# Performance work log

Measured on AMD Instinct MI355X. Metric: run time of the kernel, lower is better.

## Reference

```python
import jax, jax.numpy as jnp
import numpy as np

B, H, W = 8, 256, 256
GH, GW = 32, 32          # orig_grid_shape, = img / 2^3 after three stride-2 convs
N_STEPS = 6              # masks_num: r_x_total=3, r_y_total=3, alternating dim_stride
C_FEAT = 64
N_MASK = 4               # 4 shifted supervoxel masks summed in setup
DN = ('NHWC', 'HWIO', 'NHWC')
# deconves_importances[r_x-1]; r_x sequence over steps = 1,1,2,2,3,3
LOSS_W = (0.1, 0.1, 0.5, 0.5, 1.0, 1.0)


def _conv(x, w, b, strides=(1, 1)):
    return jax.lax.conv_general_dilated(x, w, strides, 'SAME', dimension_numbers=DN) + b


def _trio(x, w, b, strides=(1, 1)):
    # Conv_trio: conv + channel norm + gelu
    y = _conv(x, w, b, strides)
    mu = jnp.mean(y, axis=-1, keepdims=True)
    var = jnp.var(y, axis=-1, keepdims=True)
    y = (y - mu) * jax.lax.rsqrt(var + 1e-6)
    return jax.nn.gelu(y)


def setup_inputs() -> dict:
    key = jax.random.key(0)
    ks = jax.random.split(key, 8)
    s = 0.05
    w1 = jax.random.normal(ks[0], (3, 3, 1, 16), jnp.float32) * s
    w2 = jax.random.normal(ks[1], (3, 3, 16, 16), jnp.float32) * s
    w3 = jax.random.normal(ks[2], (3, 3, 16, 32), jnp.float32) * s
    w4 = jax.random.normal(ks[3], (3, 3, 32, C_FEAT), jnp.float32) * s
    up_w = jax.random.normal(ks[4], (3, 3, C_FEAT, C_FEAT), jnp.float32) * s
    mask_w = jax.random.normal(ks[5], (3, 3, C_FEAT, N_MASK), jnp.float32) * s
    b1 = jnp.zeros((16,)); b2 = jnp.zeros((16,)); b3 = jnp.zeros((32,))
    b4 = jnp.zeros((C_FEAT,)); up_b = jnp.zeros((C_FEAT,)); mask_b = jnp.zeros((N_MASK,))
    # initial supervoxel masks: sum of 4 shifted checkerboards -> per-cell grid ids
    xs = jnp.arange(GH) % 2
    ys = jnp.arange(GW) % 2
    ids = (xs[:, None] + 2 * ys[None, :]).astype(jnp.float32)  # [GH,GW] in {0,1,2,3}
    masks0 = jnp.broadcast_to(ids[None, :, :, None], (B, GH, GW, 1))
    image = jax.random.normal(ks[6], (B, H, W, 1), jnp.float32)
    return {"image": image, "dynamic_cfg": 0,
            "w1": w1, "b1": b1, "w2": w2, "b2": b2, "w3": w3, "b3": b3,
            "w4": w4, "b4": b4, "up_w": up_w, "up_b": up_b,
            "mask_w": mask_w, "mask_b": mask_b, "masks0": masks0}


def reference(image, dynamic_cfg, w1, b1, w2, b2, w3, b3, w4, b4,
              up_w, up_b, mask_w, mask_b, masks0):
    # encoder: Conv_trio(16) -> (16,s2) -> (32,s2) -> (64,s2)
    x = _trio(image, w1, b1)
    x = _trio(x, w2, b2, (2, 2))
    x = _trio(x, w3, b3, (2, 2))
    deconv_multi = _trio(x, w4, b4, (2, 2))  # [B,32,32,64]
    masks = masks0
    losses = jnp.zeros((1,), image.dtype)
    offsets = jnp.arange(N_MASK, dtype=image.dtype)
    for i in range(N_STEPS):  # fixed, structurally distinct resolutions
        dim = i % 2  # alternating dim_stride as in r_x_r_y_dim_stride
        strides = (2, 1) if dim == 0 else (1, 2)
        deconv_multi = jax.nn.gelu(
            jax.lax.conv_transpose(deconv_multi, up_w, strides, 'SAME',
                                   dimension_numbers=DN) + up_b)
        probs = jax.nn.softmax(_conv(deconv_multi, mask_w, mask_b), axis=-1)  # [B,h,w,4]
        masks = jnp.repeat(masks, 2, axis=dim + 1)
        masks = masks + 0.25 * jnp.sum(probs * offsets, axis=-1, keepdims=True)
        h, w_ = deconv_multi.shape[1], deconv_multi.shape[2]
        img_ds = image.reshape(B, h, H // h, w_, W // w_, 1).mean(axis=(2, 4))
        recon = jnp.sum(probs * offsets, axis=-1, keepdims=True) / 3.0
        entropy = -jnp.sum(probs * jnp.log(probs + 1e-8), axis=-1)
        losses = losses + LOSS_W[i] * (jnp.mean(entropy) + jnp.mean((recon - img_ds) ** 2))
    return losses, masks
```

## Files before the change

### kernel.cpp

```cpp
#include <hip/hip_runtime.h>
#include <hip/hip_bf16.h>
#include <math.h>

typedef __hip_bfloat16 bf16;
typedef float f32x4 __attribute__((ext_vector_type(4)));
typedef __bf16 bf16x8 __attribute__((ext_vector_type(8)));

#define DEV __device__ __forceinline__

DEV float to_f(float v){ return v; }
DEV float to_f(bf16 v){ return __bfloat162float(v); }
DEV bf16 f2b(float v){ return __float2bfloat16(v); }
DEV unsigned short b2u(bf16 v){ return __builtin_bit_cast(unsigned short, v); }

DEV float gelu_f(float x){
  float z = 1.5957691216057308f*(x + 0.044715f*x*x*x);
  float e = __expf(-z);
  return x * __builtin_amdgcn_rcpf(1.0f + e);
}

DEV bf16x8 load_frag(const bf16* p, bool ok){
  uint4 u = make_uint4(0u,0u,0u,0u);
  if (ok) u = *(const uint4*)p;
  return __builtin_bit_cast(bf16x8, u);
}

DEV f32x4 mfma16(bf16x8 a, uint4 b, f32x4 c){
  return __builtin_amdgcn_mfma_f32_16x16x32_bf16(a, __builtin_bit_cast(bf16x8, b), c, 0, 0, 0);
}

DEV int swz8(int blk, int n){
  return (blk & 7) * (n >> 3) + (blk >> 3);
}

DEV void dma16(const void* g, void* l){
  __builtin_amdgcn_global_load_lds(
      (const __attribute__((address_space(1))) unsigned int*)g,
      (__attribute__((address_space(3))) unsigned int*)l,
      16, 0, 0);
}

#define NSLOT 64

template<typename TIN, int CIN, int COUT, int SUB, int STRIDE, int HI, int WI>
__global__ void trio_kernel(const TIN* __restrict__ in, const float* __restrict__ w,
                            const float* __restrict__ bias, bf16* __restrict__ out){
  constexpr int HO = HI/STRIDE, WO = WI/STRIDE;
  constexpr int CO_PER = COUT/SUB;
  int gtid = blockIdx.x*blockDim.x + threadIdx.x;
  int sub = gtid % SUB;
  int pix = gtid / SUB;
  int b = pix / (HO*WO); int rem = pix % (HO*WO);
  int y = rem / WO, x = rem % WO;

  float acc[CO_PER];
  #pragma unroll
  for (int j=0;j<CO_PER;j++) acc[j]=0.f;

  for (int ky=0;ky<3;ky++){
    int iy = (STRIDE==1) ? (y+ky-1) : (2*y+ky);
    if (iy<0 || iy>=HI) continue;
    for (int kx=0;kx<3;kx++){
      int ix = (STRIDE==1) ? (x+kx-1) : (2*x+kx);
      if (ix<0 || ix>=WI) continue;
      const TIN* ip = in + ((size_t)(b*HI+iy)*WI+ix)*CIN;
      const float* wp = w + ((ky*3+kx)*CIN)*COUT + sub*CO_PER;
      #pragma unroll 4
      for (int ci=0; ci<CIN; ci++){
        float a = to_f(ip[ci]);
        const float4* w4 = (const float4*)(wp + (size_t)ci*COUT);
        #pragma unroll
        for (int j=0;j<CO_PER/4;j++){
          float4 ww = w4[j];
          acc[4*j+0] += a*ww.x; acc[4*j+1] += a*ww.y;
          acc[4*j+2] += a*ww.z; acc[4*j+3] += a*ww.w;
        }
      }
    }
  }

  float s1=0.f, s2=0.f;
  #pragma unroll
  for (int j=0;j<CO_PER;j++){
    acc[j] += bias[sub*CO_PER+j];
    s1 += acc[j]; s2 += acc[j]*acc[j];
  }
  #pragma unroll
  for (int off=1; off<SUB; off<<=1){
    s1 += __shfl_xor(s1,off,64);
    s2 += __shfl_xor(s2,off,64);
  }
  float mu  = s1*(1.0f/COUT);
  float var = s2*(1.0f/COUT) - mu*mu;
  float sc  = rsqrtf(var + 1e-6f);

  bf16* op = out + (size_t)pix*COUT + sub*CO_PER;
  #pragma unroll
  for (int j=0;j<CO_PER;j++) op[j] = f2b(gelu_f((acc[j]-mu)*sc));
}


template<int COUT>
__global__ void repack_c16(const float* __restrict__ w, bf16* __restrict__ bp){
  constexpr int NT = COUT/16;
  int v = blockIdx.x*256 + threadIdx.x;
  if (v >= 5*NT*64*8) return;
  int j = v & 7; int lane = (v>>3)&63; int idx = v>>9;
  int nt = idx % NT; int P = idx / NT;
  int m = lane & 15, quad = lane >> 4;
  int tp = quad >> 1;
  int ci = (quad & 1)*8 + j;
  int tap = 2*P + tp;
  int co = nt*16 + m;
  bp[v] = (tap < 9) ? f2b(w[((size_t)tap*16 + ci)*COUT + co]) : f2b(0.0f);
}

__global__ void repack_c32(const float* __restrict__ w, bf16* __restrict__ bp){
  int v = blockIdx.x*256 + threadIdx.x;
  if (v >= 9*4*64*8) return;
  int j = v & 7; int lane = (v>>3)&63; int idx = v>>9;
  int nt = idx & 3; int tap = idx >> 2;
  int m = lane & 15, quad = lane >> 4;
  int ci = quad*8 + j;
  int co = nt*16 + m;
  bp[v] = f2b(w[((size_t)tap*32 + ci)*64 + co]);
}

template<int CIN, int COUT, int HI, int WI>
__global__ void trio_mfma(const bf16* __restrict__ in, const bf16* __restrict__ bpack,
                          const float* __restrict__ bias, bf16* __restrict__ out){
  constexpr int HO = HI/2, WO = WI/2, NT = COUT/16;
  constexpr int TPR = WO/16;
  int lane = threadIdx.x & 63, wv = threadIdx.x >> 6;
  int wtile = blockIdx.x*4 + wv;
  int m = lane & 15, quad = lane >> 4;

  int x0 = (wtile % TPR)*16;
  int oy = (wtile / TPR) % HO;
  int b  = wtile / (TPR*HO);

  const uint4* bp4 = (const uint4*)bpack;

  f32x4 acc[NT];
  #pragma unroll
  for (int nt=0;nt<NT;nt++) acc[nt] = (f32x4){0.f,0.f,0.f,0.f};

  if constexpr (CIN == 32){
    #pragma unroll
    for (int tap=0; tap<9; tap++){
      int ky = tap/3, kx = tap%3;
      int iy = 2*oy + ky;
      int ix = 2*(x0 + m) + kx;
      bool ok = (iy < HI) && (ix < WI);
      bf16x8 a = load_frag(in + ((size_t)(b*HI+iy)*WI + ix)*32 + quad*8, ok);
      #pragma unroll
      for (int nt=0;nt<NT;nt++)
        acc[nt] = mfma16(a, bp4[(tap*NT+nt)*64 + lane], acc[nt]);
    }
  } else {
    #pragma unroll
    for (int P=0; P<5; P++){
      int tap = 2*P + (quad >> 1);
      int ky = tap/3, kx = tap - ky*3;
      int iy = 2*oy + ky;
      int ix = 2*(x0 + m) + kx;
      bool ok = (tap < 9) && (iy < HI) && (ix < WI);
      bf16x8 a = load_frag(in + ((size_t)(b*HI+iy)*WI + ix)*16 + (quad&1)*8, ok);
      #pragma unroll
      for (int nt=0;nt<NT;nt++)
        acc[nt] = mfma16(a, bp4[(P*NT+nt)*64 + lane], acc[nt]);
    }
  }

  float av[NT][4];
  float s1[4] = {0.f,0.f,0.f,0.f}, s2[4] = {0.f,0.f,0.f,0.f};
  #pragma unroll
  for (int nt=0;nt<NT;nt++){
    float bv = bias[nt*16 + m];
    #pragma unroll
    for (int r=0;r<4;r++){
      float v = acc[nt][r] + bv;
      av[nt][r] = v;
      s1[r] += v; s2[r] += v*v;
    }
  }
  #pragma unroll
  for (int r=0;r<4;r++){
    #pragma unroll
    for (int off=1; off<16; off<<=1){
      s1[r] += __shfl_xor(s1[r], off, 64);
      s2[r] += __shfl_xor(s2[r], off, 64);
    }
  }
  #pragma unroll
  for (int r=0;r<4;r++){
    float mu  = s1[r]*(1.0f/COUT);
    float var = s2[r]*(1.0f/COUT) - mu*mu;
    float sc  = rsqrtf(var + 1e-6f);
    size_t px = ((size_t)(b*HO + oy))*WO + x0 + quad*4 + r;
    #pragma unroll
    for (int nt=0;nt<NT;nt++)
      out[px*COUT + nt*16 + m] = f2b(gelu_f((av[nt][r]-mu)*sc));
  }
}

__global__ void repack_up(const float* __restrict__ w, bf16* __restrict__ bp){
  int v = blockIdx.x*256 + threadIdx.x;
  if (v >= 9*2*4*64*8) return;
  int j = v & 7; int lane = (v>>3)&63; int nt = (v>>9)&3; int c = (v>>11)&1; int tap = v>>12;
  int ci = c*32 + (lane>>4)*8 + j;
  int co = (lane&15)*4 + nt;
  bp[v] = f2b(w[(tap*64+ci)*64 + co]);
}

__global__ void repack_mask(const float* __restrict__ w, bf16* __restrict__ bp){
  int v = blockIdx.x*256 + threadIdx.x;
  if (v >= 9*2*64*8) return;
  int j = v & 7; int lane = (v>>3)&63; int c = (v>>9)&1; int tap = v>>10;
  int ci = c*32 + (lane>>4)*8 + j;
  int n = lane & 15;
  bp[v] = (n < 4) ? f2b(w[(tap*64+ci)*4 + n]) : f2b(0.0f);
}

template<int HI, int WI>
__global__ void upconv_dim0(const bf16* __restrict__ in, const bf16* __restrict__ bpack,
                            const float* __restrict__ upb, bf16* __restrict__ out){
  constexpr int HO = 2*HI, WO = WI, XT = WI/32;
  int lane = threadIdx.x & 63, wv = threadIdx.x >> 6;
  int wtile = swz8(blockIdx.x, gridDim.x)*4 + wv;
  int m = lane & 15, quad = lane >> 4;

  int x0 = (wtile % XT)*32;
  int o  = (wtile / XT) % HO;
  int b  = wtile / (XT*HO);

  int q = o >> 1;
  int stk[2], stq[2]; int nst;
  if (o & 1){ stk[0]=1; stq[0]=q; nst=1; }
  else {
    nst = 0;
    if (q >= 1){ stk[0]=0; stq[0]=q-1; nst=1; }
    stk[nst]=2; stq[nst]=q; nst++;
  }

  f32x4 acc[2][4];
  #pragma unroll
  for (int t=0;t<2;t++)
    #pragma unroll
    for (int nt=0;nt<4;nt++) acc[t][nt] = (f32x4){0.f,0.f,0.f,0.f};

  const uint4* bp4 = (const uint4*)bpack;

  #pragma unroll 1
  for (int s=0; s<nst; s++){
    int kyt = stk[s];
    const bf16* rowp = in + ((size_t)(b*HI+stq[s])*WI)*64 + quad*8;
    #pragma unroll
    for (int ut=0; ut<3; ut++){
      #pragma unroll
      for (int c=0;c<2;c++){
        int ix0 = x0 + m - 1 + ut;
        int ix1 = ix0 + 16;
        bf16x8 a0 = load_frag(rowp + (size_t)ix0*64 + c*32, ix0>=0 && ix0<WI);
        bf16x8 a1 = load_frag(rowp + (size_t)ix1*64 + c*32, ix1>=0 && ix1<WI);
        #pragma unroll
        for (int nt=0;nt<4;nt++){
          uint4 Bq = bp4[(((kyt*3+ut)*2+c)*4+nt)*64 + lane];
          acc[0][nt] = mfma16(a0, Bq, acc[0][nt]);
          acc[1][nt] = mfma16(a1, Bq, acc[1][nt]);
        }
      }
    }
  }

  float4 bv = *(const float4*)(upb + m*4);
  size_t rowbase = ((size_t)b*HO + o)*WO;
  #pragma unroll
  for (int t=0;t<2;t++){
    #pragma unroll
    for (int r=0;r<4;r++){
      int p = x0 + t*16 + quad*4 + r;
      float g0 = gelu_f(acc[t][0][r] + bv.x);
      float g1 = gelu_f(acc[t][1][r] + bv.y);
      float g2 = gelu_f(acc[t][2][r] + bv.z);
      float g3 = gelu_f(acc[t][3][r] + bv.w);
      unsigned int lo = (unsigned int)b2u(f2b(g0)) | ((unsigned int)b2u(f2b(g1))<<16);
      unsigned int hi = (unsigned int)b2u(f2b(g2)) | ((unsigned int)b2u(f2b(g3))<<16);
      *(uint2*)(out + (rowbase + p)*64 + m*4) = make_uint2(lo,hi);
    }
  }
}

template<int HI, int WI>
__global__ void __launch_bounds__(256,2)
upconv_dim0_bs(const bf16* __restrict__ in, const bf16* __restrict__ bpack,
               const float* __restrict__ upb, bf16* __restrict__ out){
  constexpr int HO = 2*HI, WO = WI, XT = WI/32;
  __shared__ __align__(16) uint4 Bsh[4608];
  int tid = threadIdx.x, lane = tid & 63, wv = tid >> 6;
  int wtile = swz8(blockIdx.x, gridDim.x)*4 + wv;
  int m = lane & 15, quad = lane >> 4;

  int x0 = (wtile % XT)*32;
  int o  = (wtile / XT) % HO;
  int b  = wtile / (XT*HO);

  {
    const uint4* gp = (const uint4*)bpack;
    #pragma unroll
    for (int k=0;k<18;k++){
      int base = (wv*18 + k)*64;
      dma16(gp + base + lane, Bsh + base);
    }
  }

  int q = o >> 1;
  int stk[2], stq[2]; int nst;
  if (o & 1){ stk[0]=1; stq[0]=q; nst=1; }
  else {
    nst = 0;
    if (q >= 1){ stk[0]=0; stq[0]=q-1; nst=1; }
    stk[nst]=2; stq[nst]=q; nst++;
  }

  f32x4 acc[2][4];
  #pragma unroll
  for (int t=0;t<2;t++)
    #pragma unroll
    for (int nt=0;nt<4;nt++) acc[t][nt] = (f32x4){0.f,0.f,0.f,0.f};

  asm volatile("s_waitcnt vmcnt(0)" ::: "memory");
  __syncthreads();

  #pragma unroll 1
  for (int s=0; s<nst; s++){
    int kyt = stk[s];
    const bf16* rowp = in + ((size_t)(b*HI+stq[s])*WI)*64 + quad*8;
    #pragma unroll
    for (int ut=0; ut<3; ut++){
      #pragma unroll
      for (int c=0;c<2;c++){
        int ix0 = x0 + m - 1 + ut;
        int ix1 = ix0 + 16;
        bf16x8 a0 = load_frag(rowp + (size_t)ix0*64 + c*32, ix0>=0 && ix0<WI);
        bf16x8 a1 = load_frag(rowp + (size_t)ix1*64 + c*32, ix1>=0 && ix1<WI);
        #pragma unroll
        for (int nt=0;nt<4;nt++){
          uint4 Bq = Bsh[(((kyt*3+ut)*2+c)*4+nt)*64 + lane];
          acc[0][nt] = mfma16(a0, Bq, acc[0][nt]);
          acc[1][nt] = mfma16(a1, Bq, acc[1][nt]);
        }
      }
    }
  }

  float4 bv = *(const float4*)(upb + m*4);
  size_t rowbase = ((size_t)b*HO + o)*WO;
  #pragma unroll
  for (int t=0;t<2;t++){
    #pragma unroll
    for (int r=0;r<4;r++){
      int p = x0 + t*16 + quad*4 + r;
      float g0 = gelu_f(acc[t][0][r] + bv.x);
      float g1 = gelu_f(acc[t][1][r] + bv.y);
      float g2 = gelu_f(acc[t][2][r] + bv.z);
      float g3 = gelu_f(acc[t][3][r] + bv.w);
      unsigned int lo = (unsigned int)b2u(f2b(g0)) | ((unsigned int)b2u(f2b(g1))<<16);
      unsigned int hi = (unsigned int)b2u(f2b(g2)) | ((unsigned int)b2u(f2b(g3))<<16);
      *(uint2*)(out + (rowbase + p)*64 + m*4) = make_uint2(lo,hi);
    }
  }
}

template<int HI, int WI>
__global__ void upconv_dim1(const bf16* __restrict__ in, const bf16* __restrict__ bpack,
                            const float* __restrict__ upb, bf16* __restrict__ out){
  constexpr int HO = HI, WO = 2*WI, QT = WI/16;
  int lane = threadIdx.x & 63, wv = threadIdx.x >> 6;
  int wtile = swz8(blockIdx.x, gridDim.x)*4 + wv;
  int m = lane & 15, quad = lane >> 4;

  int q0 = (wtile % QT)*16;
  int y  = (wtile / QT) % HI;
  int b  = wtile / (QT*HI);

  f32x4 ae[4], ao[4];
  #pragma unroll
  for (int nt=0;nt<4;nt++){ ae[nt]=(f32x4){0.f,0.f,0.f,0.f}; ao[nt]=(f32x4){0.f,0.f,0.f,0.f}; }

  const uint4* bp4 = (const uint4*)bpack;

  #pragma unroll 1
  for (int ky=0; ky<3; ky++){
    int iy = y + ky - 1;
    if (iy < 0 || iy >= HI) continue;
    const bf16* rowp = in + ((size_t)(b*HI+iy)*WI)*64 + quad*8;
    #pragma unroll
    for (int c=0;c<2;c++){
      int qa = q0 + m;
      bf16x8 Au = load_frag(rowp + (size_t)qa*64 + c*32, true);
      bf16x8 As = load_frag(rowp + (size_t)(qa-1)*64 + c*32, qa >= 1);
      #pragma unroll
      for (int nt=0;nt<4;nt++){
        uint4 B0 = bp4[(((ky*3+0)*2+c)*4+nt)*64 + lane];
        uint4 B1 = bp4[(((ky*3+1)*2+c)*4+nt)*64 + lane];
        uint4 B2 = bp4[(((ky*3+2)*2+c)*4+nt)*64 + lane];
        ae[nt] = mfma16(As, B0, ae[nt]);
        ae[nt] = mfma16(Au, B2, ae[nt]);
        ao[nt] = mfma16(Au, B1, ao[nt]);
      }
    }
  }

  float4 bv = *(const float4*)(upb + m*4);
  size_t rowbase = ((size_t)b*HO + y)*WO;
  #pragma unroll
  for (int r=0;r<4;r++){
    int qq = q0 + quad*4 + r;
    {
      float g0 = gelu_f(ae[0][r] + bv.x);
      float g1 = gelu_f(ae[1][r] + bv.y);
      float g2 = gelu_f(ae[2][r] + bv.z);
      float g3 = gelu_f(ae[3][r] + bv.w);
      unsigned int lo = (unsigned int)b2u(f2b(g0)) | ((unsigned int)b2u(f2b(g1))<<16);
      unsigned int hi = (unsigned int)b2u(f2b(g2)) | ((unsigned int)b2u(f2b(g3))<<16);
      *(uint2*)(out + (rowbase + 2*qq)*64 + m*4) = make_uint2(lo,hi);
    }
    {
      float g0 = gelu_f(ao[0][r] + bv.x);
      float g1 = gelu_f(ao[1][r] + bv.y);
      float g2 = gelu_f(ao[2][r] + bv.z);
      float g3 = gelu_f(ao[3][r] + bv.w);
      unsigned int lo = (unsigned int)b2u(f2b(g0)) | ((unsigned int)b2u(f2b(g1))<<16);
      unsigned int hi = (unsigned int)b2u(f2b(g2)) | ((unsigned int)b2u(f2b(g3))<<16);
      *(uint2*)(out + (rowbase + 2*qq+1)*64 + m*4) = make_uint2(lo,hi);
    }
  }
}

template<int HI, int WI>
__global__ void __launch_bounds__(256,2)
upconv_dim1_bs(const bf16* __restrict__ in, const bf16* __restrict__ bpack,
               const float* __restrict__ upb, bf16* __restrict__ out){
  constexpr int HO = HI, WO = 2*WI, QT = WI/16;
  __shared__ __align__(16) uint4 Bsh[4608];
  int tid = threadIdx.x, lane = tid & 63, wv = tid >> 6;
  int wtile = swz8(blockIdx.x, gridDim.x)*4 + wv;
  int m = lane & 15, quad = lane >> 4;

  int q0 = (wtile % QT)*16;
  int y  = ((wtile / QT) % (HI/2)) * 2;
  int b  = wtile / (QT*(HI/2));

  {
    const uint4* gp = (const uint4*)bpack;
    #pragma unroll
    for (int k=0;k<18;k++){
      int base = (wv*18 + k)*64;
      dma16(gp + base + lane, Bsh + base);
    }
  }

  int qa = q0 + m;

  bf16x8 Afr[4][2][2];
  #pragma unroll
  for (int i4=0;i4<4;i4++){
    int iy = y + i4 - 1;
    bool ok = (iy>=0) && (iy<HI);
    const bf16* rowp = in + ((size_t)(b*HI+iy)*WI)*64 + quad*8;
    #pragma unroll
    for (int c=0;c<2;c++){
      Afr[i4][c][0] = load_frag(rowp + (size_t)qa*64 + c*32, ok);
      Afr[i4][c][1] = load_frag(rowp + (size_t)(qa-1)*64 + c*32, ok && qa >= 1);
    }
  }

  asm volatile("s_waitcnt vmcnt(0)" ::: "memory");
  __syncthreads();

  f32x4 ae[2][4], ao[2][4];
  #pragma unroll
  for (int r=0;r<2;r++)
    #pragma unroll
    for (int nt=0;nt<4;nt++){ ae[r][nt]=(f32x4){0.f,0.f,0.f,0.f}; ao[r][nt]=(f32x4){0.f,0.f,0.f,0.f}; }

  #pragma unroll
  for (int ky=0; ky<3; ky++){
    #pragma unroll
    for (int c=0;c<2;c++){
      #pragma unroll
      for (int nt=0;nt<4;nt++){
        uint4 B0 = Bsh[(((ky*3+0)*2+c)*4+nt)*64 + lane];
        uint4 B1 = Bsh[(((ky*3+1)*2+c)*4+nt)*64 + lane];
        uint4 B2 = Bsh[(((ky*3+2)*2+c)*4+nt)*64 + lane];
        #pragma unroll
        for (int r=0;r<2;r++){
          ae[r][nt] = mfma16(Afr[ky+r][c][1], B0, ae[r][nt]);
          ae[r][nt] = mfma16(Afr[ky+r][c][0], B2, ae[r][nt]);
          ao[r][nt] = mfma16(Afr[ky+r][c][0], B1, ao[r][nt]);
        }
      }
    }
  }

  float4 bv = *(const float4*)(upb + m*4);
  #pragma unroll
  for (int r2=0;r2<2;r2++){
    size_t rowbase = ((size_t)b*HO + y + r2)*WO;
    #pragma unroll
    for (int r=0;r<4;r++){
      int qq = q0 + quad*4 + r;
      {
        float g0 = gelu_f(ae[r2][0][r] + bv.x);
        float g1 = gelu_f(ae[r2][1][r] + bv.y);
        float g2 = gelu_f(ae[r2][2][r] + bv.z);
        float g3 = gelu_f(ae[r2][3][r] + bv.w);
        unsigned int lo = (unsigned int)b2u(f2b(g0)) | ((unsigned int)b2u(f2b(g1))<<16);
        unsigned int hi = (unsigned int)b2u(f2b(g2)) | ((unsigned int)b2u(f2b(g3))<<16);
        *(uint2*)(out + (rowbase + 2*qq)*64 + m*4) = make_uint2(lo,hi);
      }
      {
        float g0 = gelu_f(ao[r2][0][r] + bv.x);
        float g1 = gelu_f(ao[r2][1][r] + bv.y);
        float g2 = gelu_f(ao[r2][2][r] + bv.z);
        float g3 = gelu_f(ao[r2][3][r] + bv.w);
        unsigned int lo = (unsigned int)b2u(f2b(g0)) | ((unsigned int)b2u(f2b(g1))<<16);
        unsigned int hi = (unsigned int)b2u(f2b(g2)) | ((unsigned int)b2u(f2b(g3))<<16);
        *(uint2*)(out + (rowbase + 2*qq+1)*64 + m*4) = make_uint2(lo,hi);
      }
    }
  }
}

template<int STEP, int DIM, int HH, int WW, int TILES>
__global__ void maskloss_mfma(const bf16* __restrict__ feat, const bf16* __restrict__ mpack,
                              const float* __restrict__ mb, const float* __restrict__ img,
                              const float* __restrict__ masks_in, float* __restrict__ masks_out,
                              float* __restrict__ accbuf){
  __shared__ float llog[4][64][4];
  __shared__ float red[4][2];
  int lane = threadIdx.x & 63;
  int wv   = threadIdx.x >> 6;
  int wtile = swz8(blockIdx.x, gridDim.x)*4 + wv;
  int m = lane & 15, quad = lane >> 4;

  constexpr int TPR = WW/(16*TILES);
  int x0 = (wtile % TPR)*(16*TILES);
  int y  = (wtile / TPR) % HH;
  int b  = wtile / (TPR*HH);

  const uint4* bp4 = (const uint4*)mpack;

  #pragma unroll 1
  for (int t=0; t<TILES; t++){
    f32x4 acc4 = (f32x4){0.f,0.f,0.f,0.f};
    #pragma unroll
    for (int c=0;c<2;c++){
      bf16x8 afr[9];
      #pragma unroll
      for (int ky=0; ky<3; ky++){
        int iy = y + ky - 1;
        bool rowok = (iy >= 0) && (iy < HH);
        const bf16* rowp = feat + ((size_t)(b*HH+iy)*WW)*64 + quad*8 + c*32;
        #pragma unroll
        for (int kx=0; kx<3; kx++){
          int ix = x0 + t*16 + m + kx - 1;
          bool ok = rowok && (ix >= 0) && (ix < WW);
          afr[ky*3+kx] = load_frag(rowp + (size_t)ix*64, ok);
        }
      }
      #pragma unroll
      for (int tap=0; tap<9; tap++){
        uint4 bb = bp4[(tap*2+c)*64 + lane];
        acc4 = mfma16(afr[tap], bb, acc4);
      }
    }
    if (m < 4){
      #pragma unroll
      for (int r=0;r<4;r++) llog[wv][t*16 + quad*4 + r][m] = acc4[r] + mb[m];
    }
  }
  __syncthreads();

  float ent = 0.f, mse = 0.f;
  if (lane < 16*TILES){
    int p = lane; int xx = x0 + p;
    float l0 = llog[wv][p][0], l1 = llog[wv][p][1];
    float l2 = llog[wv][p][2], l3 = llog[wv][p][3];
    float mx = fmaxf(fmaxf(l0,l1), fmaxf(l2,l3));
    float d0=l0-mx, d1=l1-mx, d2=l2-mx, d3=l3-mx;
    float e0=__expf(d0), e1=__expf(d1), e2=__expf(d2), e3=__expf(d3);
    float S = e0+e1+e2+e3;
    float inv = __builtin_amdgcn_rcpf(S);
    float sval = (e1 + 2.f*e2 + 3.f*e3)*inv;

    constexpr int HM = (DIM==0)? HH/2 : HH;
    constexpr int WM = (DIM==0)? WW : WW/2;
    int my = (DIM==0)? (y>>1) : y;
    int mxi = (DIM==1)? (xx>>1) : xx;
    float mv = masks_in[((size_t)b*HM + my)*WM + mxi];
    masks_out[((size_t)b*HH + y)*WW + xx] = mv + 0.25f*sval;

    ent = __logf(S) - (e0*d0 + e1*d1 + e2*d2 + e3*d3)*inv;

    constexpr int FH = 256/HH, FW = 256/WW;
    float isum = 0.f;
    const float* ib = img + ((size_t)b*256 + y*FH)*256 + xx*FW;
    #pragma unroll
    for (int dy=0; dy<FH; dy++)
      #pragma unroll
      for (int dx=0; dx<FW; dx++) isum += ib[dy*256+dx];
    float img_ds = isum * (1.0f/(FH*FW));
    float d = sval*(1.0f/3.0f) - img_ds;
    mse = d*d;
  }

  #pragma unroll
  for (int off=1; off<64; off<<=1){
    ent += __shfl_xor(ent, off, 64);
    mse += __shfl_xor(mse, off, 64);
  }
  if (lane == 0){ red[wv][0] = ent; red[wv][1] = mse; }
  __syncthreads();
  if (threadIdx.x == 0){
    float e  = red[0][0] + red[1][0] + red[2][0] + red[3][0];
    float ms = red[0][1] + red[1][1] + red[2][1] + red[3][1];
    int slot = blockIdx.x & (NSLOT-1);
    atomicAdd(accbuf + (2*STEP  )*NSLOT + slot, e);
    atomicAdd(accbuf + (2*STEP+1)*NSLOT + slot, ms);
  }
}

template<int STEP, int DIM, int HH, int WW, int ROWS>
__global__ void maskloss_lds(const bf16* __restrict__ feat, const bf16* __restrict__ mpack,
                             const float* __restrict__ mb, const float* __restrict__ img,
                             const float* __restrict__ masks_in, float* __restrict__ masks_out,
                             float* __restrict__ accbuf){
  constexpr int NBrow = WW/64;
  constexpr int PITCH = 9216;
  constexpr int NR = ROWS + 2;
  constexpr int WPR = 4/ROWS;
  __shared__ __align__(16) char smem[NR*PITCH];
  __shared__ float llog[4][ROWS][16][4];
  __shared__ float red[4][2];
  int tid = threadIdx.x;
  int lane = tid & 63, wv = tid >> 6;
  int bi = swz8(blockIdx.x, gridDim.x);
  int x0 = (bi % NBrow)*64;
  int y0 = ((bi / NBrow) % (HH/ROWS)) * ROWS;
  int b  = bi / (NBrow*(HH/ROWS));
  int m = lane & 15, quad = lane >> 4;
  int lanesw = ((lane ^ (lane>>3)) << 4);

  int r_w   = wv / WPR;
  int xbase = (wv % WPR) * (16*ROWS);
  int yw    = y0 + r_w;

  for (int k = wv; k < NR*9; k += 4){
    int r = k/9, coff = (k%9)*1024;
    int iy = y0 + r - 1;
    if (iy < 0 || iy >= HH) continue;
    const char* g = (const char*)(feat + ((size_t)(b*HH+iy)*WW + x0 - 1)*64)
                    + coff + lanesw;
    dma16(g, smem + r*PITCH + coff);
  }
  asm volatile("s_waitcnt vmcnt(0)" ::: "memory");
  __syncthreads();
  if (x0 == 0 && tid < 32*NR)
    ((float*)(smem + (tid>>5)*PITCH))[tid & 31] = 0.f;
  if (x0 + 64 == WW && tid >= 128 && tid < 128 + 32*NR){
    int t = tid - 128;
    ((float*)(smem + (t>>5)*PITCH + 65*128))[t & 31] = 0.f;
  }
  __syncthreads();

  const uint4* bp4 = (const uint4*)mpack;
  #pragma unroll
  for (int t=0; t<ROWS; t++){
    f32x4 accA = (f32x4){0.f,0.f,0.f,0.f};
    f32x4 accB = (f32x4){0.f,0.f,0.f,0.f};
    #pragma unroll
    for (int ky=0; ky<3; ky++){
      int iyw = yw + ky - 1;
      if (iyw < 0 || iyw >= HH) continue;
      const char* rowl = smem + (size_t)(r_w + ky)*PITCH;
      #pragma unroll
      for (int kx=0; kx<3; kx++){
        int lp = xbase + t*16 + m + kx;
        const char* pl = rowl + (size_t)lp*128;
        int xw = (lp & 7) << 4;
        bf16x8 a0 = __builtin_bit_cast(bf16x8, *(const uint4*)(pl + ((quad*16     ) ^ xw)));
        bf16x8 a1 = __builtin_bit_cast(bf16x8, *(const uint4*)(pl + ((quad*16 + 64) ^ xw)));
        uint4 b0 = bp4[((ky*3+kx)*2+0)*64 + lane];
        uint4 b1 = bp4[((ky*3+kx)*2+1)*64 + lane];
        accA = mfma16(a0, b0, accA);
        accB = mfma16(a1, b1, accB);
      }
    }
    if (m < 4){
      #pragma unroll
      for (int r=0;r<4;r++) llog[wv][t][quad*4+r][m] = accA[r] + accB[r] + mb[m];
    }
  }
  __syncthreads();

  float ent = 0.f, mse = 0.f;
  if (lane < 16*ROWS){
    int t = lane >> 4;
    int p = lane & 15;
    int xx = x0 + xbase + t*16 + p;
    float l0 = llog[wv][t][p][0], l1 = llog[wv][t][p][1];
    float l2 = llog[wv][t][p][2], l3 = llog[wv][t][p][3];
    float mx = fmaxf(fmaxf(l0,l1), fmaxf(l2,l3));
    float d0=l0-mx, d1=l1-mx, d2=l2-mx, d3=l3-mx;
    float e0=__expf(d0), e1=__expf(d1), e2=__expf(d2), e3=__expf(d3);
    float S = e0+e1+e2+e3;
    float inv = __builtin_amdgcn_rcpf(S);
    float sval = (e1 + 2.f*e2 + 3.f*e3)*inv;

    constexpr int HM = (DIM==0)? HH/2 : HH;
    constexpr int WM = (DIM==0)? WW : WW/2;
    int my = (DIM==0)? (yw>>1) : yw;
    int mxi = (DIM==1)? (xx>>1) : xx;
    float mv = masks_in[((size_t)b*HM + my)*WM + mxi];
    masks_out[((size_t)b*HH + yw)*WW + xx] = mv + 0.25f*sval;

    ent = __logf(S) - (e0*d0 + e1*d1 + e2*d2 + e3*d3)*inv;

    constexpr int FH = 256/HH, FW = 256/WW;
    float isum = 0.f;
    const float* ib = img + ((size_t)b*256 + yw*FH)*256 + xx*FW;
    #pragma unroll
    for (int dy=0; dy<FH; dy++)
      #pragma unroll
      for (int dx=0; dx<FW; dx++) isum += ib[dy*256+dx];
    float img_ds = isum * (1.0f/(FH*FW));
    float d = sval*(1.0f/3.0f) - img_ds;
    mse = d*d;
  }

  #pragma unroll
  for (int off=1; off<64; off<<=1){
    ent += __shfl_xor(ent, off, 64);
    mse += __shfl_xor(mse, off, 64);
  }
  if (lane == 0){ red[wv][0] = ent; red[wv][1] = mse; }
  __syncthreads();
  if (threadIdx.x == 0){
    float e  = red[0][0] + red[1][0] + red[2][0] + red[3][0];
    float ms = red[0][1] + red[1][1] + red[2][1] + red[3][1];
    int slot = blockIdx.x & (NSLOT-1);
    atomicAdd(accbuf + (2*STEP  )*NSLOT + slot, e);
    atomicAdd(accbuf + (2*STEP+1)*NSLOT + slot, ms);
  }
}

__global__ void finalize_kernel(const float* __restrict__ acc, float* __restrict__ out){
  int lane = threadIdx.x & 63;
  float v[12];
  #pragma unroll
  for (int i=0;i<12;i++){
    float x = acc[i*NSLOT + lane];
    #pragma unroll
    for (int off=1; off<64; off<<=1) x += __shfl_xor(x, off, 64);
    v[i] = x;
  }
  if (lane == 0){
    const float lw[6] = {0.1f,0.1f,0.5f,0.5f,1.0f,1.0f};
    const float nn[6] = {16384.f,32768.f,65536.f,131072.f,262144.f,524288.f};
    float L=0.f;
    for (int i=0;i<6;i++) L += lw[i]*((v[2*i] + v[2*i+1])/nn[i]);
    out[0]=L;
  }
}

extern "C" void kernel_launch(void* const* d_in, const int* in_sizes, int n_in,
                              void* d_out, int out_size, void* d_ws, size_t ws_size,
                              hipStream_t stream){
  const float* image  = (const float*)d_in[0];
  const float* w1=(const float*)d_in[2];  const float* b1=(const float*)d_in[3];
  const float* w2=(const float*)d_in[4];  const float* b2=(const float*)d_in[5];
  const float* w3=(const float*)d_in[6];  const float* b3=(const float*)d_in[7];
  const float* w4=(const float*)d_in[8];  const float* b4=(const float*)d_in[9];
  const float* upw=(const float*)d_in[10];const float* upb=(const float*)d_in[11];
  const float* mw=(const float*)d_in[12]; const float* mb=(const float*)d_in[13];
  const float* masks0=(const float*)d_in[14];
  float* out = (float*)d_out;

  char* ws = (char*)d_ws;
  size_t off = 0;
  auto alloc = [&](size_t bytes)->char*{
    char* p = ws + off; off += (bytes + 255) & ~(size_t)255; return p;
  };
  bf16* enc1  = (bf16*)alloc((size_t)8*256*256*16*2);
  bf16* enc2  = (bf16*)alloc((size_t)8*128*128*16*2);
  bf16* enc3  = (bf16*)alloc((size_t)8*64*64*32*2);
  bf16* featA = (bf16*)alloc((size_t)8*256*256*64*2);
  bf16* featB = (bf16*)alloc((size_t)8*256*128*64*2);
  float* mbA  = (float*)alloc((size_t)8*256*128*4);
  float* mbB  = (float*)alloc((size_t)8*128*128*4);
  bf16* packU = (bf16*)alloc((size_t)9*2*4*64*8*2);
  bf16* packM = (bf16*)alloc((size_t)9*2*64*8*2);
  bf16* packT2= (bf16*)alloc((size_t)5*1*64*8*2);
  bf16* packT3= (bf16*)alloc((size_t)5*2*64*8*2);
  bf16* packT4= (bf16*)alloc((size_t)9*4*64*8*2);
  float* acc  = (float*)alloc(12*NSLOT*sizeof(float));

  hipMemsetAsync(acc, 0, 12*NSLOT*sizeof(float), stream);

  repack_up  <<<144,256,0,stream>>>(upw, packU);
  repack_mask<<< 36,256,0,stream>>>(mw,  packM);
  repack_c16<16><<<10,256,0,stream>>>(w2, packT2);
  repack_c16<32><<<20,256,0,stream>>>(w3, packT3);
  repack_c32    <<<72,256,0,stream>>>(w4, packT4);

  trio_kernel<float,1,16,1,1,256,256><<<8*256*256/256,256,0,stream>>>(image,w1,b1,enc1);
  trio_mfma<16,16,256,256><<<8*128*128/16/4,256,0,stream>>>(enc1,packT2,b2,enc2);
  trio_mfma<16,32,128,128><<<8*64*64/16/4,256,0,stream>>>(enc2,packT3,b3,enc3);
  trio_mfma<32,64,64,64><<<8*32*32/16/4,256,0,stream>>>(enc3,packT4,b4,featA);

  upconv_dim0<32,32><<<128,256,0,stream>>>(featA,packU,upb,featB);
  maskloss_mfma<0,0,64,32,2><<<128,256,0,stream>>>(featB,packM,mb,image,masks0,mbA,acc);
  upconv_dim1<64,32><<<256,256,0,stream>>>(featB,packU,upb,featA);
  maskloss_lds<1,1,64,64,1><<<512,256,0,stream>>>(featA,packM,mb,image,mbA,mbB,acc);
  upconv_dim0_bs<64,64><<<512,256,0,stream>>>(featA,packU,upb,featB);
  maskloss_lds<2,0,128,64,1><<<1024,256,0,stream>>>(featB,packM,mb,image,mbB,mbA,acc);
  upconv_dim1_bs<128,64><<<512,256,0,stream>>>(featB,packU,upb,featA);
  maskloss_lds<3,1,128,128,2><<<1024,256,0,stream>>>(featA,packM,mb,image,mbA,mbB,acc);
  upconv_dim0_bs<128,128><<<2048,256,0,stream>>>(featA,packU,upb,featB);
  maskloss_lds<4,0,256,128,2><<<2048,256,0,stream>>>(featB,packM,mb,image,mbB,mbA,acc);
  upconv_dim1_bs<256,128><<<2048,256,0,stream>>>(featB,packU,upb,featA);
  maskloss_lds<5,1,256,256,2><<<4096,256,0,stream>>>(featA,packM,mb,image,mbA,out+1,acc);

  finalize_kernel<<<1,64,0,stream>>>(acc,out);
}
```

Baseline: 351.4 us.

## Use 8-wave blocks for the largest upconv and mask-loss stages, merge repack kernels

Adds 512-thread variants of the upconv (dim0 and dim1) and mask-loss kernels for the two largest resolutions. Each block stages the packed weights in LDS once and shares them across 8 waves instead of 4, which halves the per-block weight staging traffic and the block count. The five weight repack launches are merged into a single kernel to cut launch overhead. The larger blocks may lower occupancy flexibility, and the mask-loss kernel now stages a taller 6-row halo tile.

```diff
diff --git a/kernel.cpp b/kernel.cpp
--- a/kernel.cpp
+++ b/kernel.cpp
@@ -99,33 +99,6 @@
   for (int j=0;j<CO_PER;j++) op[j] = f2b(gelu_f((acc[j]-mu)*sc));
 }
 
-
-template<int COUT>
-__global__ void repack_c16(const float* __restrict__ w, bf16* __restrict__ bp){
-  constexpr int NT = COUT/16;
-  int v = blockIdx.x*256 + threadIdx.x;
-  if (v >= 5*NT*64*8) return;
-  int j = v & 7; int lane = (v>>3)&63; int idx = v>>9;
-  int nt = idx % NT; int P = idx / NT;
-  int m = lane & 15, quad = lane >> 4;
-  int tp = quad >> 1;
-  int ci = (quad & 1)*8 + j;
-  int tap = 2*P + tp;
-  int co = nt*16 + m;
-  bp[v] = (tap < 9) ? f2b(w[((size_t)tap*16 + ci)*COUT + co]) : f2b(0.0f);
-}
-
-__global__ void repack_c32(const float* __restrict__ w, bf16* __restrict__ bp){
-  int v = blockIdx.x*256 + threadIdx.x;
-  if (v >= 9*4*64*8) return;
-  int j = v & 7; int lane = (v>>3)&63; int idx = v>>9;
-  int nt = idx & 3; int tap = idx >> 2;
-  int m = lane & 15, quad = lane >> 4;
-  int ci = quad*8 + j;
-  int co = nt*16 + m;
-  bp[v] = f2b(w[((size_t)tap*32 + ci)*64 + co]);
-}
-
 template<int CIN, int COUT, int HI, int WI>
 __global__ void trio_mfma(const bf16* __restrict__ in, const bf16* __restrict__ bpack,
                           const float* __restrict__ bias, bf16* __restrict__ out){
@@ -204,22 +177,50 @@
   }
 }
 
-__global__ void repack_up(const float* __restrict__ w, bf16* __restrict__ bp){
+__global__ void repack_all(const float* __restrict__ upw, const float* __restrict__ mw,
+                           const float* __restrict__ w2, const float* __restrict__ w3,
+                           const float* __restrict__ w4,
+                           bf16* __restrict__ bpU, bf16* __restrict__ bpM,
+                           bf16* __restrict__ bpT2, bf16* __restrict__ bpT3,
+                           bf16* __restrict__ bpT4){
   int v = blockIdx.x*256 + threadIdx.x;
-  if (v >= 9*2*4*64*8) return;
-  int j = v & 7; int lane = (v>>3)&63; int nt = (v>>9)&3; int c = (v>>11)&1; int tap = v>>12;
-  int ci = c*32 + (lane>>4)*8 + j;
-  int co = (lane&15)*4 + nt;
-  bp[v] = f2b(w[(tap*64+ci)*64 + co]);
-}
-
-__global__ void repack_mask(const float* __restrict__ w, bf16* __restrict__ bp){
-  int v = blockIdx.x*256 + threadIdx.x;
-  if (v >= 9*2*64*8) return;
-  int j = v & 7; int lane = (v>>3)&63; int c = (v>>9)&1; int tap = v>>10;
-  int ci = c*32 + (lane>>4)*8 + j;
-  int n = lane & 15;
-  bp[v] = (n < 4) ? f2b(w[(tap*64+ci)*4 + n]) : f2b(0.0f);
+  if (v < 36864){
+    int u = v;
+    int j = u & 7; int lane = (u>>3)&63; int nt = (u>>9)&3; int c = (u>>11)&1; int tap = u>>12;
+    int ci = c*32 + (lane>>4)*8 + j;
+    int co = (lane&15)*4 + nt;
+    bpU[u] = f2b(upw[(tap*64+ci)*64 + co]);
+  } else if (v < 46080){
+    int u = v - 36864;
+    int j = u & 7; int lane = (u>>3)&63; int c = (u>>9)&1; int tap = u>>10;
+    int ci = c*32 + (lane>>4)*8 + j;
+    int n = lane & 15;
+    bpM[u] = (n < 4) ? f2b(mw[(tap*64+ci)*4 + n]) : f2b(0.0f);
+  } else if (v < 48640){
+    int u = v - 46080;
+    int j = u & 7; int lane = (u>>3)&63; int P = u>>9;
+    int m = lane & 15, quad = lane >> 4;
+    int ci = (quad & 1)*8 + j;
+    int tap = 2*P + (quad >> 1);
+    bpT2[u] = (tap < 9) ? f2b(w2[((size_t)tap*16 + ci)*16 + m]) : f2b(0.0f);
+  } else if (v < 53760){
+    int u = v - 48640;
+    int j = u & 7; int lane = (u>>3)&63; int idx = u>>9;
+    int nt = idx % 2; int P = idx / 2;
+    int m = lane & 15, quad = lane >> 4;
+    int ci = (quad & 1)*8 + j;
+    int tap = 2*P + (quad >> 1);
+    int co = nt*16 + m;
+    bpT3[u] = (tap < 9) ? f2b(w3[((size_t)tap*16 + ci)*32 + co]) : f2b(0.0f);
+  } else if (v < 72192){
+    int u = v - 53760;
+    int j = u & 7; int lane = (u>>3)&63; int idx = u>>9;
+    int nt = idx & 3; int tap = idx >> 2;
+    int m = lane & 15, quad = lane >> 4;
+    int ci = quad*8 + j;
+    int co = nt*16 + m;
+    bpT4[u] = f2b(w4[((size_t)tap*32 + ci)*64 + co]);
+  }
 }
 
 template<int HI, int WI>
@@ -373,6 +374,87 @@
 }
 
 template<int HI, int WI>
+__global__ void __launch_bounds__(512,4)
+upconv_dim0_bs8(const bf16* __restrict__ in, const bf16* __restrict__ bpack,
+                const float* __restrict__ upb, bf16* __restrict__ out){
+  constexpr int HO = 2*HI, WO = WI, XT = WI/32;
+  __shared__ __align__(16) uint4 Bsh[4608];
+  int tid = threadIdx.x, lane = tid & 63, wv = tid >> 6;
+  int wtile = swz8(blockIdx.x, gridDim.x)*8 + wv;
+  int m = lane & 15, quad = lane >> 4;
+
+  int x0 = (wtile % XT)*32;
+  int o  = (wtile / XT) % HO;
+  int b  = wtile / (XT*HO);
+
+  {
+    const uint4* gp = (const uint4*)bpack;
+    #pragma unroll
+    for (int k=0;k<9;k++){
+      int base = (wv*9 + k)*64;
+      dma16(gp + base + lane, Bsh + base);
+    }
+  }
+
+  int q = o >> 1;
+  int stk[2], stq[2]; int nst;
+  if (o & 1){ stk[0]=1; stq[0]=q; nst=1; }
+  else {
+    nst = 0;
+    if (q >= 1){ stk[0]=0; stq[0]=q-1; nst=1; }
+    stk[nst]=2; stq[nst]=q; nst++;
+  }
+
+  f32x4 acc[2][4];
+  #pragma unroll
+  for (int t=0;t<2;t++)
+    #pragma unroll
+    for (int nt=0;nt<4;nt++) acc[t][nt] = (f32x4){0.f,0.f,0.f,0.f};
+
+  asm volatile("s_waitcnt vmcnt(0)" ::: "memory");
+  __syncthreads();
+
+  #pragma unroll 1
+  for (int s=0; s<nst; s++){
+    int kyt = stk[s];
+    const bf16* rowp = in + ((size_t)(b*HI+stq[s])*WI)*64 + quad*8;
+    #pragma unroll
+    for (int ut=0; ut<3; ut++){
+      #pragma unroll
+      for (int c=0;c<2;c++){
+        int ix0 = x0 + m - 1 + ut;
+        int ix1 = ix0 + 16;
+        bf16x8 a0 = load_frag(rowp + (size_t)ix0*64 + c*32, ix0>=0 && ix0<WI);
+        bf16x8 a1 = load_frag(rowp + (size_t)ix1*64 + c*32, ix1>=0 && ix1<WI);
+        #pragma unroll
+        for (int nt=0;nt<4;nt++){
+          uint4 Bq = Bsh[(((kyt*3+ut)*2+c)*4+nt)*64 + lane];
+          acc[0][nt] = mfma16(a0, Bq, acc[0][nt]);
+          acc[1][nt] = mfma16(a1, Bq, acc[1][nt]);
+        }
+      }
+    }
+  }
+
+  float4 bv = *(const float4*)(upb + m*4);
+  size_t rowbase = ((size_t)b*HO + o)*WO;
+  #pragma unroll
+  for (int t=0;t<2;t++){
+    #pragma unroll
+    for (int r=0;r<4;r++){
+      int p = x0 + t*16 + quad*4 + r;
+      float g0 = gelu_f(acc[t][0][r] + bv.x);
+      float g1 = gelu_f(acc[t][1][r] + bv.y);
+      float g2 = gelu_f(acc[t][2][r] + bv.z);
+      float g3 = gelu_f(acc[t][3][r] + bv.w);
+      unsigned int lo = (unsigned int)b2u(f2b(g0)) | ((unsigned int)b2u(f2b(g1))<<16);
+      unsigned int hi = (unsigned int)b2u(f2b(g2)) | ((unsigned int)b2u(f2b(g3))<<16);
+      *(uint2*)(out + (rowbase + p)*64 + m*4) = make_uint2(lo,hi);
+    }
+  }
+}
+
+template<int HI, int WI>
 __global__ void upconv_dim1(const bf16* __restrict__ in, const bf16* __restrict__ bpack,
                             const float* __restrict__ upb, bf16* __restrict__ out){
   constexpr int HO = HI, WO = 2*WI, QT = WI/16;
@@ -457,6 +539,101 @@
     #pragma unroll
     for (int k=0;k<18;k++){
       int base = (wv*18 + k)*64;
+      dma16(gp + base + lane, Bsh + base);
+    }
+  }
+
+  int qa = q0 + m;
+
+  bf16x8 Afr[4][2][2];
+  #pragma unroll
+  for (int i4=0;i4<4;i4++){
+    int iy = y + i4 - 1;
+    bool ok = (iy>=0) && (iy<HI);
+    const bf16* rowp = in + ((size_t)(b*HI+iy)*WI)*64 + quad*8;
+    #pragma unroll
+    for (int c=0;c<2;c++){
+      Afr[i4][c][0] = load_frag(rowp + (size_t)qa*64 + c*32, ok);
+      Afr[i4][c][1] = load_frag(rowp + (size_t)(qa-1)*64 + c*32, ok && qa >= 1);
+    }
+  }
+
+  asm volatile("s_waitcnt vmcnt(0)" ::: "memory");
+  __syncthreads();
+
+  f32x4 ae[2][4], ao[2][4];
+  #pragma unroll
+  for (int r=0;r<2;r++)
+    #pragma unroll
+    for (int nt=0;nt<4;nt++){ ae[r][nt]=(f32x4){0.f,0.f,0.f,0.f}; ao[r][nt]=(f32x4){0.f,0.f,0.f,0.f}; }
+
+  #pragma unroll
+  for (int ky=0; ky<3; ky++){
+    #pragma unroll
+    for (int c=0;c<2;c++){
+      #pragma unroll
+      for (int nt=0;nt<4;nt++){
+        uint4 B0 = Bsh[(((ky*3+0)*2+c)*4+nt)*64 + lane];
+        uint4 B1 = Bsh[(((ky*3+1)*2+c)*4+nt)*64 + lane];
+        uint4 B2 = Bsh[(((ky*3+2)*2+c)*4+nt)*64 + lane];
+        #pragma unroll
+        for (int r=0;r<2;r++){
+          ae[r][nt] = mfma16(Afr[ky+r][c][1], B0, ae[r][nt]);
+          ae[r][nt] = mfma16(Afr[ky+r][c][0], B2, ae[r][nt]);
+          ao[r][nt] = mfma16(Afr[ky+r][c][0], B1, ao[r][nt]);
+        }
+      }
+    }
+  }
+
+  float4 bv = *(const float4*)(upb + m*4);
+  #pragma unroll
+  for (int r2=0;r2<2;r2++){
+    size_t rowbase = ((size_t)b*HO + y + r2)*WO;
+    #pragma unroll
+    for (int r=0;r<4;r++){
+      int qq = q0 + quad*4 + r;
+      {
+        float g0 = gelu_f(ae[r2][0][r] + bv.x);
+        float g1 = gelu_f(ae[r2][1][r] + bv.y);
+        float g2 = gelu_f(ae[r2][2][r] + bv.z);
+        float g3 = gelu_f(ae[r2][3][r] + bv.w);
+        unsigned int lo = (unsigned int)b2u(f2b(g0)) | ((unsigned int)b2u(f2b(g1))<<16);
+        unsigned int hi = (unsigned int)b2u(f2b(g2)) | ((unsigned int)b2u(f2b(g3))<<16);
+        *(uint2*)(out + (rowbase + 2*qq)*64 + m*4) = make_uint2(lo,hi);
+      }
+      {
+        float g0 = gelu_f(ao[r2][0][r] + bv.x);
+        float g1 = gelu_f(ao[r2][1][r] + bv.y);
+        float g2 = gelu_f(ao[r2][2][r] + bv.z);
+        float g3 = gelu_f(ao[r2][3][r] + bv.w);
+        unsigned int lo = (unsigned int)b2u(f2b(g0)) | ((unsigned int)b2u(f2b(g1))<<16);
+        unsigned int hi = (unsigned int)b2u(f2b(g2)) | ((unsigned int)b2u(f2b(g3))<<16);
+        *(uint2*)(out + (rowbase + 2*qq+1)*64 + m*4) = make_uint2(lo,hi);
+      }
+    }
+  }
+}
+
+template<int HI, int WI>
+__global__ void __launch_bounds__(512,4)
+upconv_dim1_bs8(const bf16* __restrict__ in, const bf16* __restrict__ bpack,
+                const float* __restrict__ upb, bf16* __restrict__ out){
+  constexpr int HO = HI, WO = 2*WI, QT = WI/16;
+  __shared__ __align__(16) uint4 Bsh[4608];
+  int tid = threadIdx.x, lane = tid & 63, wv = tid >> 6;
+  int wtile = swz8(blockIdx.x, gridDim.x)*8 + wv;
+  int m = lane & 15, quad = lane >> 4;
+
+  int q0 = (wtile % QT)*16;
+  int y  = ((wtile / QT) % (HI/2)) * 2;
+  int b  = wtile / (QT*(HI/2));
+
+  {
+    const uint4* gp = (const uint4*)bpack;
+    #pragma unroll
+    for (int k=0;k<9;k++){
+      int base = (wv*9 + k)*64;
       dma16(gp + base + lane, Bsh + base);
     }
   }
@@ -756,6 +933,131 @@
   }
 }
 
+template<int STEP, int DIM, int HH, int WW>
+__global__ void __launch_bounds__(512,4)
+maskloss_lds8(const bf16* __restrict__ feat, const bf16* __restrict__ mpack,
+              const float* __restrict__ mb, const float* __restrict__ img,
+              const float* __restrict__ masks_in, float* __restrict__ masks_out,
+              float* __restrict__ accbuf){
+  constexpr int NBrow = WW/64;
+  constexpr int PITCH = 9216;
+  constexpr int NR = 6;
+  __shared__ __align__(16) char smem[NR*PITCH];
+  __shared__ float llog[8][2][16][4];
+  __shared__ float red[8][2];
+  int tid = threadIdx.x;
+  int lane = tid & 63, wv = tid >> 6;
+  int bi = swz8(blockIdx.x, gridDim.x);
+  int x0 = (bi % NBrow)*64;
+  int y0 = ((bi / NBrow) % (HH/4)) * 4;
+  int b  = bi / (NBrow*(HH/4));
+  int m = lane & 15, quad = lane >> 4;
+  int lanesw = ((lane ^ (lane>>3)) << 4);
+
+  int r_w   = wv >> 1;
+  int xbase = (wv & 1) * 32;
+  int yw    = y0 + r_w;
+
+  for (int k = wv; k < NR*9; k += 8){
+    int r = k/9, coff = (k%9)*1024;
+    int iy = y0 + r - 1;
+    if (iy < 0 || iy >= HH) continue;
+    const char* g = (const char*)(feat + ((size_t)(b*HH+iy)*WW + x0 - 1)*64)
+                    + coff + lanesw;
+    dma16(g, smem + r*PITCH + coff);
+  }
+  asm volatile("s_waitcnt vmcnt(0)" ::: "memory");
+  __syncthreads();
+  if (x0 == 0 && tid < 32*NR)
+    ((float*)(smem + (tid>>5)*PITCH))[tid & 31] = 0.f;
+  if (x0 + 64 == WW && tid >= 256 && tid < 256 + 32*NR){
+    int t = tid - 256;
+    ((float*)(smem + (t>>5)*PITCH + 65*128))[t & 31] = 0.f;
+  }
+  __syncthreads();
+
+  const uint4* bp4 = (const uint4*)mpack;
+  #pragma unroll
+  for (int t=0; t<2; t++){
+    f32x4 accA = (f32x4){0.f,0.f,0.f,0.f};
+    f32x4 accB = (f32x4){0.f,0.f,0.f,0.f};
+    #pragma unroll
+    for (int ky=0; ky<3; ky++){
+      int iyw = yw + ky - 1;
+      if (iyw < 0 || iyw >= HH) continue;
+      const char* rowl = smem + (size_t)(r_w + ky)*PITCH;
+      #pragma unroll
+      for (int kx=0; kx<3; kx++){
+        int lp = xbase + t*16 + m + kx;
+        const char* pl = rowl + (size_t)lp*128;
+        int xw = (lp & 7) << 4;
+        bf16x8 a0 = __builtin_bit_cast(bf16x8, *(const uint4*)(pl + ((quad*16     ) ^ xw)));
+        bf16x8 a1 = __builtin_bit_cast(bf16x8, *(const uint4*)(pl + ((quad*16 + 64) ^ xw)));
+        uint4 b0 = bp4[((ky*3+kx)*2+0)*64 + lane];
+        uint4 b1 = bp4[((ky*3+kx)*2+1)*64 + lane];
+        accA = mfma16(a0, b0, accA);
+        accB = mfma16(a1, b1, accB);
+      }
+    }
+    if (m < 4){
+      #pragma unroll
+      for (int r=0;r<4;r++) llog[wv][t][quad*4+r][m] = accA[r] + accB[r] + mb[m];
+    }
+  }
+  __syncthreads();
+
+  float ent = 0.f, mse = 0.f;
+  if (lane < 32){
+    int t = lane >> 4;
+    int p = lane & 15;
+    int xx = x0 + xbase + t*16 + p;
+    float l0 = llog[wv][t][p][0], l1 = llog[wv][t][p][1];
+    float l2 = llog[wv][t][p][2], l3 = llog[wv][t][p][3];
+    float mx = fmaxf(fmaxf(l0,l1), fmaxf(l2,l3));
+    float d0=l0-mx, d1=l1-mx, d2=l2-mx, d3=l3-mx;
+    float e0=__expf(d0), e1=__expf(d1), e2=__expf(d2), e3=__expf(d3);
+    float S = e0+e1+e2+e3;
+    float inv = __builtin_amdgcn_rcpf(S);
+    float sval = (e1 + 2.f*e2 + 3.f*e3)*inv;
+
+    constexpr int HM = (DIM==0)? HH/2 : HH;
+    constexpr int WM = (DIM==0)? WW : WW/2;
+    int my = (DIM==0)? (yw>>1) : yw;
+    int mxi = (DIM==1)? (xx>>1) : xx;
+    float mv = masks_in[((size_t)b*HM + my)*WM + mxi];
+    masks_out[((size_t)b*HH + yw)*WW + xx] = mv + 0.25f*sval;
+
+    ent = __logf(S) - (e0*d0 + e1*d1 + e2*d2 + e3*d3)*inv;
+
+    constexpr int FH = 256/HH, FW = 256/WW;
+    float isum = 0.f;
+    const float* ib = img + ((size_t)b*256 + yw*FH)*256 + xx*FW;
+    #pragma unroll
+    for (int dy=0; dy<FH; dy++)
+      #pragma unroll
+      for (int dx=0; dx<FW; dx++) isum += ib[dy*256+dx];
+    float img_ds = isum * (1.0f/(FH*FW));
+    float d = sval*(1.0f/3.0f) - img_ds;
+    mse = d*d;
+  }
+
+  #pragma unroll
+  for (int off=1; off<64; off<<=1){
+    ent += __shfl_xor(ent, off, 64);
+    mse += __shfl_xor(mse, off, 64);
+  }
+  if (lane == 0){ red[wv][0] = ent; red[wv][1] = mse; }
+  __syncthreads();
+  if (threadIdx.x == 0){
+    float e = 0.f, ms = 0.f;
+    #pragma unroll
+    for (int i=0;i<8;i++){ e += red[i][0]; ms += red[i][1]; }
+    int slot = blockIdx.x & (NSLOT-1);
+    atomicAdd(accbuf + (2*STEP  )*NSLOT + slot, e);
+    atomicAdd(accbuf + (2*STEP+1)*NSLOT + slot, ms);
+  }
+}
+
 __global__ void finalize_kernel(const float* __restrict__ acc, float* __restrict__ out){
   int lane = threadIdx.x & 63;
   float v[12];
@@ -809,11 +1111,8 @@
 
   hipMemsetAsync(acc, 0, 12*NSLOT*sizeof(float), stream);
 
-  repack_up  <<<144,256,0,stream>>>(upw, packU);
-  repack_mask<<< 36,256,0,stream>>>(mw,  packM);
-  repack_c16<16><<<10,256,0,stream>>>(w2, packT2);
-  repack_c16<32><<<20,256,0,stream>>>(w3, packT3);
-  repack_c32    <<<72,256,0,stream>>>(w4, packT4);
+  repack_all<<<282,256,0,stream>>>(upw, mw, w2, w3, w4,
+                                   packU, packM, packT2, packT3, packT4);
 
   trio_kernel<float,1,16,1,1,256,256><<<8*256*256/256,256,0,stream>>>(image,w1,b1,enc1);
   trio_mfma<16,16,256,256><<<8*128*128/16/4,256,0,stream>>>(enc1,packT2,b2,enc2);
@@ -828,10 +1127,10 @@
   maskloss_lds<2,0,128,64,1><<<1024,256,0,stream>>>(featB,packM,mb,image,mbB,mbA,acc);
   upconv_dim1_bs<128,64><<<512,256,0,stream>>>(featB,packU,upb,featA);
   maskloss_lds<3,1,128,128,2><<<1024,256,0,stream>>>(featA,packM,mb,image,mbA,mbB,acc);
-  upconv_dim0_bs<128,128><<<2048,256,0,stream>>>(featA,packU,upb,featB);
-  maskloss_lds<4,0,256,128,2><<<2048,256,0,stream>>>(featB,packM,mb,image,mbB,mbA,acc);
-  upconv_dim1_bs<256,128><<<2048,256,0,stream>>>(featB,packU,upb,featA);
-  maskloss_lds<5,1,256,256,2><<<4096,256,0,stream>>>(featA,packM,mb,image,mbA,out+1,acc);
+  upconv_dim0_bs8<128,128><<<1024,512,0,stream>>>(featA,packU,upb,featB);
+  maskloss_lds8<4,0,256,128><<<1024,512,0,stream>>>(featB,packM,mb,image,mbB,mbA,acc);
+  upconv_dim1_bs8<256,128><<<1024,512,0,stream>>>(featB,packU,upb,featA);
+  maskloss_lds8<5,1,256,256><<<2048,512,0,stream>>>(featA,packM,mb,image,mbA,out+1,acc);
 
   finalize_kernel<<<1,64,0,stream>>>(acc,out);
 }
```

Result: faster. 328.8 us, median of 2 (-6.4%).
